# Performance work log

Hardware: AMD Instinct MI355X
Metric: run time of the kernel (lower is better)

## Reference

```python
import jax, jax.numpy as jnp
import numpy as np

B, T = 64, 256
CHAR_V, CHAR_D = 8000, 128
WORD_V, WORD_D = 100000, 300
POS_V, POS_D = 30, 64
SPO_D = 20
D = CHAR_D + WORD_D + POS_D + SPO_D  # 512
L, H, KD, VD, INNER = 4, 8, 64, 64, 2048
C = 25  # num tag classes


def _layer_norm(x, g, b, eps=1e-5):
    m = jnp.mean(x, axis=-1, keepdims=True)
    v = jnp.mean(jnp.square(x - m), axis=-1, keepdims=True)
    return (x - m) * jax.lax.rsqrt(v + eps) * g + b


def setup_inputs() -> dict:
    key = jax.random.key(0)
    ks = jax.random.split(key, 40)
    s = 0.05
    n = lambda k, shp, sc=0.05: jax.random.normal(k, shp, jnp.float32) * sc
    return {
        "char": jax.random.randint(ks[0], (B, T), 0, CHAR_V),
        "word": jax.random.randint(ks[1], (B, T), 0, WORD_V),
        "pos": jax.random.randint(ks[2], (B, T), 0, POS_V),
        "spo": jax.random.normal(ks[3], (B, SPO_D), jnp.float32),
        "seq_len": jax.random.randint(ks[4], (B,), 1, T + 1),
        "tag": jax.random.randint(ks[5], (B, T), 0, C),
        "char_table": n(ks[6], (CHAR_V, CHAR_D)),
        "word_table": n(ks[7], (WORD_V, WORD_D)),
        "pos_table": n(ks[8], (POS_V, POS_D)),
        "ln0_g": jnp.ones((D,), jnp.float32),
        "ln0_b": jnp.zeros((D,), jnp.float32),
        "Wq": n(ks[9], (L, D, H * KD)), "bq": jnp.zeros((L, H * KD), jnp.float32),
        "Wk": n(ks[10], (L, D, H * KD)), "bk": jnp.zeros((L, H * KD), jnp.float32),
        "Wv": n(ks[11], (L, D, H * VD)), "bv": jnp.zeros((L, H * VD), jnp.float32),
        "Wo": n(ks[12], (L, H * VD, D)), "bo": jnp.zeros((L, D), jnp.float32),
        "ln1_g": jnp.ones((L, D), jnp.float32), "ln1_b": jnp.zeros((L, D), jnp.float32),
        "W1": n(ks[13], (L, D, INNER)), "b1": jnp.zeros((L, INNER), jnp.float32),
        "W2": n(ks[14], (L, INNER, D)), "b2": jnp.zeros((L, D), jnp.float32),
        "ln2_g": jnp.ones((L, D), jnp.float32), "ln2_b": jnp.zeros((L, D), jnp.float32),
        "Wout": n(ks[15], (D, C)), "bout": jnp.zeros((C,), jnp.float32),
        "trans": n(ks[16], (C, C)),
    }


def _forward(spo, char_table, word_table, pos_table, ln0_g, ln0_b,
             Wq, bq, Wk, bk, Wv, bv, Wo, bo, ln1_g, ln1_b,
             W1, b1, W2, b2, ln2_g, ln2_b, Wout, bout, trans,
             char, word, pos, seq_len, tag):
    # mask[b,t] = t < seq_len[b]
    mask = (jnp.arange(T)[None, :] < seq_len[:, None]).astype(jnp.float32)  # [B,T]

    # embed + concat + layernorm (dropout in eval mode = identity)
    x = jnp.concatenate([
        char_table[char], word_table[word], pos_table[pos],
        jnp.broadcast_to(spo[:, None, :], (B, T, SPO_D)),
    ], axis=-1)  # [B,T,D]
    x = _layer_norm(x, ln0_g, ln0_b)

    neg_inf = jnp.finfo(x.dtype).min
    key_ok = mask[:, None, None, :] > 0  # [B,1,1,T] key padding mask
    scale = jnp.sqrt(jnp.asarray(KD, x.dtype))
    for l in range(L):
        q = (x @ Wq[l] + bq[l]).reshape(B, T, H, KD).transpose(0, 2, 1, 3)
        k = (x @ Wk[l] + bk[l]).reshape(B, T, H, KD).transpose(0, 2, 1, 3)
        v = (x @ Wv[l] + bv[l]).reshape(B, T, H, VD).transpose(0, 2, 1, 3)
        scores = jnp.einsum('bhqd,bhkd->bhqk', q, k) / scale
        scores = jnp.where(key_ok, scores, neg_inf)
        attn = jax.nn.softmax(scores, axis=-1)
        ctx = jnp.einsum('bhqk,bhkd->bhqd', attn, v).transpose(0, 2, 1, 3).reshape(B, T, H * VD)
        att_out = ctx @ Wo[l] + bo[l]
        h1 = _layer_norm(att_out + x, ln1_g[l], ln1_b[l])
        ff = jax.nn.relu(h1 @ W1[l] + b1[l]) @ W2[l] + b2[l]
        x = _layer_norm(ff + h1, ln2_g[l], ln2_b[l]) * mask[:, :, None]

    logits = x @ Wout + bout  # [B,T,C]

    # ---- CRF negative log likelihood (include_start_end_trans=False) ----
    lg = logits.transpose(1, 0, 2)  # [T,B,C]
    m = mask.T                      # [T,B]

    def step(alpha, inp):
        emit, mt = inp  # emit [B,C], mt [B]
        tmp = alpha[:, :, None] + trans[None, :, :] + emit[:, None, :]  # [B,C,C]
        new = jax.nn.logsumexp(tmp, axis=1)
        alpha = jnp.where(mt[:, None] > 0, new, alpha)
        return alpha, None

    alpha, _ = jax.lax.scan(step, lg[0], (lg[1:], m[1:]))
    log_z = jax.nn.logsumexp(alpha, axis=-1)  # [B]

    tags_t = tag.T  # [T,B]
    emit_gold = jnp.take_along_axis(lg, tags_t[:, :, None], axis=-1)[..., 0] * m  # [T,B]
    trans_gold = trans[tags_t[:-1], tags_t[1:]] * m[1:]  # [T-1,B]
    gold = emit_gold.sum(0) + trans_gold.sum(0)  # [B]

    return jnp.mean(log_z - gold)


def reference(char, word, pos, spo, seq_len, tag, char_table, word_table, pos_table,
              ln0_g, ln0_b, Wq, bq, Wk, bk, Wv, bv, Wo, bo, ln1_g, ln1_b,
              W1, b1, W2, b2, ln2_g, ln2_b, Wout, bout, trans):
    return _forward(spo, char_table, word_table, pos_table, ln0_g, ln0_b,
                    Wq, bq, Wk, bk, Wv, bv, Wo, bo, ln1_g, ln1_b,
                    W1, b1, W2, b2, ln2_g, ln2_b, Wout, bout, trans,
                    char, word, pos, seq_len, tag)
```

## Files before the change

### kernel.cpp

```cpp
#include <hip/hip_runtime.h>
#include <cmath>

namespace {

constexpr int LT = 4;
constexpr int BB = 64;
constexpr int TT = 256;
constexpr int DD = 512;
constexpr int HH = 8;
constexpr int DH = 64;
constexpr int FF = 2048;
constexpr int CC = 25;
constexpr int M_ALL = BB * TT;
constexpr size_t MB = 1024 * 1024;

typedef __attribute__((ext_vector_type(8))) short short8;
typedef __attribute__((ext_vector_type(4))) short short4_;
typedef __attribute__((ext_vector_type(4))) float f32x4;
typedef __attribute__((ext_vector_type(4))) _Float16 half4;

__device__ __forceinline__ float b2f(unsigned short u) {
  union { unsigned int i; float f; } x; x.i = ((unsigned int)u) << 16; return x.f;
}
__device__ __forceinline__ unsigned short f2b(float f) {
  union { float f; unsigned int i; } x; x.f = f;
  unsigned int r = x.i + 0x7FFFu + ((x.i >> 16) & 1u);
  return (unsigned short)(r >> 16);
}
__device__ __forceinline__ float rdlane(float v, int l) {
  union { float f; unsigned int i; } x; x.f = v;
  x.i = (unsigned int)__builtin_amdgcn_readlane((int)x.i, l);
  return x.f;
}
__device__ __forceinline__ void gl_lds16(const void* g, void* l) {
  __builtin_amdgcn_global_load_lds(
      (const __attribute__((address_space(1))) unsigned int*)g,
      (__attribute__((address_space(3))) unsigned int*)l, 16, 0, 0);
}
__device__ __forceinline__ float wredsum(float v) {
#pragma unroll
  for (int o = 32; o > 0; o >>= 1) v += __shfl_xor(v, o, 64);
  return v;
}

__global__ __launch_bounds__(64) void prefix_k(const int* __restrict__ sl,
                                               int* __restrict__ boff) {
  const int l = threadIdx.x;
  int s = sl[l];
#pragma unroll
  for (int o = 1; o < 64; o <<= 1) {
    const int u = __shfl_up(s, o, 64);
    if (l >= o) s += u;
  }
  boff[l + 1] = s;
  if (l == 0) boff[0] = 0;
}

__global__ __launch_bounds__(256) void rowmap_k(const int* __restrict__ sl,
                                                const int* __restrict__ boff,
                                                int* __restrict__ rowmap) {
  const int b = blockIdx.x, t = threadIdx.x;
  if (t < sl[b]) rowmap[boff[b] + t] = (b << 8) | t;
}

template <int NSRC>
__global__ __launch_bounds__(256) void wconv_k(const float* __restrict__ in0,
                                               const float* __restrict__ in1,
                                               const float* __restrict__ in2,
                                               unsigned short* __restrict__ out,
                                               int K, int N, size_t lstride,
                                               size_t sstride) {
  __shared__ float ts[64][65];
  const int k0 = blockIdx.x * 64, n0 = blockIdx.y * 64;
  const float* in = in0;
  if constexpr (NSRC == 3) {
    const int s = blockIdx.z / LT;
    in = (s == 0) ? in0 : (s == 1 ? in1 : in2);
    in += (size_t)(blockIdx.z % LT) * K * N;
    out += (size_t)(blockIdx.z % LT) * lstride + (size_t)(blockIdx.z / LT) * sstride;
  } else {
    in += (size_t)blockIdx.z * K * N;
    out += (size_t)blockIdx.z * lstride;
  }
  const int tid = threadIdx.x;
  for (int i = tid; i < 1024; i += 256) {
    const int r = i >> 4, c4 = i & 15;
    const float4 f = *(const float4*)&in[(size_t)(k0 + r) * N + n0 + c4 * 4];
    ts[r][c4 * 4 + 0] = f.x; ts[r][c4 * 4 + 1] = f.y;
    ts[r][c4 * 4 + 2] = f.z; ts[r][c4 * 4 + 3] = f.w;
  }
  __syncthreads();
  const int n_r = tid >> 2, kc = (tid & 3) * 16;
  short8 v0, v1;
#pragma unroll
  for (int j = 0; j < 8; ++j) {
    v0[j] = (short)f2b(ts[kc + j][n_r]);
    v1[j] = (short)f2b(ts[kc + 8 + j][n_r]);
  }
  unsigned short* op = out + (size_t)(n0 + n_r) * K + k0 + kc;
  *(short8*)op = v0;
  *(short8*)(op + 8) = v1;
}

__global__ __launch_bounds__(256) void embed_ln0_k(
    const int* __restrict__ ch, const int* __restrict__ wd, const int* __restrict__ ps,
    const float* __restrict__ spo, const float* __restrict__ ctab,
    const float* __restrict__ wtab, const float* __restrict__ ptab,
    const float* __restrict__ g, const float* __restrict__ be,
    const int* __restrict__ sl, const int* __restrict__ boff,
    unsigned short* __restrict__ xc) {
  const int row = blockIdx.x * 4 + (threadIdx.x >> 6);
  const int b = row >> 8, t = row & 255;
  if (t >= sl[b]) return;
  const int orow = boff[b] + t;
  const int lane = threadIdx.x & 63;
  const int ci = ch[row], wi = wd[row], pi = ps[row];
  float v[8];
#pragma unroll
  for (int j = 0; j < 2; ++j) {
    const int d = j * 256 + lane * 4;
    float4 f;
    if (d < 128)      f = *(const float4*)&ctab[(size_t)ci * 128 + d];
    else if (d < 428) f = *(const float4*)&wtab[(size_t)wi * 300 + (d - 128)];
    else if (d < 492) f = *(const float4*)&ptab[(size_t)pi * 64 + (d - 428)];
    else              f = *(const float4*)&spo[(size_t)b * 20 + (d - 492)];
    v[j * 4 + 0] = f.x; v[j * 4 + 1] = f.y; v[j * 4 + 2] = f.z; v[j * 4 + 3] = f.w;
  }
  float s = 0.f;
#pragma unroll
  for (int i = 0; i < 8; ++i) s += v[i];
  const float mean = wredsum(s) * (1.0f / 512.0f);
  float vs = 0.f;
#pragma unroll
  for (int i = 0; i < 8; ++i) { const float d = v[i] - mean; vs += d * d; }
  const float rstd = rsqrtf(wredsum(vs) * (1.0f / 512.0f) + 1e-5f);
#pragma unroll
  for (int j = 0; j < 2; ++j) {
    const int d = j * 256 + lane * 4;
    const float4 gv = *(const float4*)&g[d];
    const float4 bv = *(const float4*)&be[d];
    short4_ ob;
    ob[0] = (short)f2b((v[j * 4 + 0] - mean) * rstd * gv.x + bv.x);
    ob[1] = (short)f2b((v[j * 4 + 1] - mean) * rstd * gv.y + bv.y);
    ob[2] = (short)f2b((v[j * 4 + 2] - mean) * rstd * gv.z + bv.z);
    ob[3] = (short)f2b((v[j * 4 + 3] - mean) * rstd * gv.w + bv.w);
    *(short4_*)&xc[(size_t)orow * DD + d] = ob;
  }
}

template <int EPI, int TM>
__global__ __launch_bounds__(256) void gemm_mfma(
    const unsigned short* __restrict__ A, const unsigned short* __restrict__ Bt,
    const float* __restrict__ bias, const float* __restrict__ bias2,
    const float* __restrict__ bias3, const unsigned short* __restrict__ res,
    const int* __restrict__ Mptr, const int* __restrict__ rowmap,
    void* __restrict__ outv, void* __restrict__ out2v, void* __restrict__ out3v,
    int M, int N, int K) {
  constexpr int MI = TM / 32;
  const int Mp = Mptr[0];
  const int m0 = blockIdx.y * TM, n0 = blockIdx.x * 128;
  if (m0 >= Mp) return;
  __shared__ unsigned short As[TM * 64];
  __shared__ unsigned short Bs[128 * 64];
  const int tid = threadIdx.x;
  const int wid = tid >> 6, lane = tid & 63;
  const int wr = wid >> 1, wc = wid & 1;
  const int cl = lane & 15, rg = lane >> 4;
  f32x4 acc[MI][4];
#pragma unroll
  for (int i = 0; i < MI; ++i)
#pragma unroll
    for (int j = 0; j < 4; ++j) acc[i][j] = (f32x4){0.f, 0.f, 0.f, 0.f};

  const int rbase = tid >> 3, sl = tid & 7;
  const int sc = 8 * (sl ^ (rbase & 7));

  for (int k0 = 0; k0 < K; k0 += 64) {
    if (k0) __syncthreads();
#pragma unroll
    for (int i = 0; i < TM / 32; ++i) {
      const int r = i * 32 + rbase;
      gl_lds16(A + (size_t)(m0 + r) * K + k0 + sc, (char*)As + (i * 256 + tid) * 16);
    }
#pragma unroll
    for (int i = 0; i < 4; ++i) {
      const int r = i * 32 + rbase;
      gl_lds16(Bt + (size_t)(n0 + r) * K + k0 + sc, (char*)Bs + (i * 256 + tid) * 16);
    }
    __syncthreads();
#pragma unroll
    for (int ks = 0; ks < 2; ++ks) {
      short8 a[MI], b[4];
      const int kbyte = ks * 64 + rg * 16;
#pragma unroll
      for (int f = 0; f < MI; ++f) {
        const int am = wr * (TM / 2) + f * 16 + cl;
        a[f] = *(const short8*)((const char*)As + am * 128 + (kbyte ^ ((am & 7) << 4)));
      }
#pragma unroll
      for (int f = 0; f < 4; ++f) {
        const int bn = wc * 64 + f * 16 + cl;
        b[f] = *(const short8*)((const char*)Bs + bn * 128 + (kbyte ^ ((bn & 7) << 4)));
      }
#pragma unroll
      for (int mi = 0; mi < MI; ++mi)
#pragma unroll
        for (int ni = 0; ni < 4; ++ni)
          acc[mi][ni] = __builtin_amdgcn_mfma_f32_16x16x32_bf16(a[mi], b[ni],
                                                                acc[mi][ni], 0, 0, 0);
    }
  }

  int rm[MI][4];
  if constexpr (EPI == 5) {
#pragma unroll
    for (int mi = 0; mi < MI; ++mi) {
      const int mb_ = m0 + wr * (TM / 2) + mi * 16 + rg * 4;
#pragma unroll
      for (int i = 0; i < 4; ++i)
        rm[mi][i] = (mb_ + i < Mp) ? rowmap[mb_ + i] : -1;
    }
  }

#pragma unroll
  for (int ni = 0; ni < 4; ++ni) {
    const int n = n0 + wc * 64 + ni * 16 + cl;
    float bv;
    if constexpr (EPI == 5) {
      bv = (n < 512) ? bias[n] : (n < 1024 ? bias2[n - 512] : bias3[n - 1024]);
    } else {
      bv = bias[n];
    }
#pragma unroll
    for (int mi = 0; mi < MI; ++mi) {
      if constexpr (EPI == 5) {
        const int hh = (n >> 6) & 7, d = n & 63;
        if (n < 1024) {
          unsigned short* outp = (unsigned short*)((n < 512) ? outv : out2v);
#pragma unroll
          for (int i = 0; i < 4; ++i) {
            const int rmv = rm[mi][i];
            if (rmv >= 0) {
              const int bb = rmv >> 8, tt = rmv & 255;
              outp[(((size_t)(bb * HH + hh) * TT + tt) << 6) + d] =
                  f2b(acc[mi][ni][i] + bv);
            }
          }
        } else {
          const int rm0 = rm[mi][0];
          if (rm0 >= 0 && rm[mi][3] == rm0 + 3) {
            half4 pk;
#pragma unroll
            for (int i = 0; i < 4; ++i) pk[i] = (_Float16)(acc[mi][ni][i] + bv);
            *(half4*)((_Float16*)out3v +
                      ((((size_t)((rm0 >> 8) * HH + hh) * DH + d) << 8) + (rm0 & 255))) = pk;
          } else {
#pragma unroll
            for (int i = 0; i < 4; ++i) {
              const int rmv = rm[mi][i];
              if (rmv >= 0)
                ((_Float16*)out3v)[(((size_t)((rmv >> 8) * HH + hh) * DH + d) << 8) +
                                   (rmv & 255)] = (_Float16)(acc[mi][ni][i] + bv);
            }
          }
        }
      } else {
#pragma unroll
        for (int i = 0; i < 4; ++i) {
          const int m = m0 + wr * (TM / 2) + mi * 16 + rg * 4 + i;
          const float v = acc[mi][ni][i] + bv;
          if constexpr (EPI == 1) {
            ((unsigned short*)outv)[(size_t)m * N + n] = f2b(fmaxf(v, 0.f));
          } else if constexpr (EPI == 7) {
            ((unsigned short*)outv)[(size_t)m * N + n] =
                f2b(v + b2f(res[(size_t)m * N + n]));
          }
        }
      }
    }
  }
}

__global__ __launch_bounds__(256) void attn_mfma_k(
    const unsigned short* __restrict__ qb, const unsigned short* __restrict__ kbp,
    const _Float16* __restrict__ vtp, const int* __restrict__ seq_len,
    const int* __restrict__ boff, unsigned short* __restrict__ cb) {
  __shared__ unsigned short Ks[256 * 64];
  __shared__ _Float16 Vs[64 * 256];
  __shared__ unsigned short Os[64 * 64];
  const int bh = blockIdx.x;
  const int b = bh >> 3, h = bh & 7;
  const int tid = threadIdx.x;
  const int wid = tid >> 6, lane = tid & 63;
  const int cl = lane & 15, rg = lane >> 4;
  const int len = seq_len[b];
  const int off = boff[b];

  {
    const int r = tid >> 3, sl = tid & 7;
#pragma unroll
    for (int i = 0; i < 8; ++i) {
      if (i * 32 < len) {
        const int row = i * 32 + r;
        gl_lds16(kbp + ((size_t)bh * TT + row) * DH + 8 * (sl ^ (row & 7)),
                 (char*)Ks + (i * 256 + tid) * 16);
      }
    }
#pragma unroll
    for (int i = 0; i < 8; ++i) {
      const int u = i * 256 + tid;
      const int vrow = u >> 5, vsl = u & 31;
      gl_lds16(vtp + ((size_t)bh * DH + vrow) * TT + 8 * (vsl ^ (vrow & 7)),
               (char*)Vs + u * 16);
    }
  }
  __syncthreads();

  for (int qt4 = 0; qt4 < 4; ++qt4) {
    if (qt4 * 64 >= len) break;
    f32x4 o[4];
#pragma unroll
    for (int db = 0; db < 4; ++db) o[db] = (f32x4){0.f, 0.f, 0.f, 0.f};
    {
      const int q0 = qt4 * 64 + wid * 16;
      short8 bqf[2];
      const unsigned short* qp = qb + ((size_t)bh * TT + q0 + cl) * DH + rg * 8;
      bqf[0] = *(const short8*)qp;
      bqf[1] = *(const short8*)(qp + 32);
      f32x4 s[16];
#pragma unroll
      for (int kk = 0; kk < 16; ++kk) {
        s[kk] = (f32x4){0.f, 0.f, 0.f, 0.f};
        if (kk * 16 < len) {
          const int row = kk * 16 + cl;
          const char* base = (const char*)Ks + row * 128;
          const int sw = (row & 7) << 4;
          const short8 a0 = *(const short8*)(base + ((rg * 16) ^ sw));
          const short8 a1 = *(const short8*)(base + ((64 + rg * 16) ^ sw));
          s[kk] = __builtin_amdgcn_mfma_f32_16x16x32_bf16(a0, bqf[0], s[kk], 0, 0, 0);
          s[kk] = __builtin_amdgcn_mfma_f32_16x16x32_bf16(a1, bqf[1], s[kk], 0, 0, 0);
        }
      }
      float mx = -3.0e38f;
#pragma unroll
      for (int kk = 0; kk < 16; ++kk)
        if (kk * 16 < len) {
#pragma unroll
          for (int i = 0; i < 4; ++i) {
            float v = s[kk][i] * 0.125f;
            v = (kk * 16 + rg * 4 + i < len) ? v : -3.0e38f;
            s[kk][i] = v;
            mx = fmaxf(mx, v);
          }
        }
      mx = fmaxf(mx, __shfl_xor(mx, 16, 64));
      mx = fmaxf(mx, __shfl_xor(mx, 32, 64));
      float lsum = 0.f;
#pragma unroll
      for (int kk = 0; kk < 16; ++kk)
        if (kk * 16 < len) {
#pragma unroll
          for (int i = 0; i < 4; ++i) {
            const float p = __expf(s[kk][i] - mx);
            s[kk][i] = p;
            lsum += p;
          }
        }
      lsum += __shfl_xor(lsum, 16, 64);
      lsum += __shfl_xor(lsum, 32, 64);
      const float rl = 1.0f / lsum;
#pragma unroll
      for (int kk = 0; kk < 16; ++kk)
        if (kk * 16 < len) {
          half4 bp;
#pragma unroll
          for (int i = 0; i < 4; ++i) bp[i] = (_Float16)(s[kk][i] * rl);
#pragma unroll
          for (int db = 0; db < 4; ++db) {
            const int vrow = db * 16 + cl;
            const int byte = kk * 32 + rg * 8;
            const half4 a = *(const half4*)((const char*)Vs + vrow * 512 +
                              ((byte & ~15) ^ ((vrow & 7) << 4)) + (byte & 15));
            o[db] = __builtin_amdgcn_mfma_f32_16x16x16f16(a, bp, o[db], 0, 0, 0);
          }
        }
    }
    __syncthreads();
    {
      const int orow = wid * 16 + cl;
      char* obase = (char*)Os + orow * 128;
      const int sw = (orow & 7) << 4;
#pragma unroll
      for (int db = 0; db < 4; ++db) {
        short4_ pk;
#pragma unroll
        for (int i = 0; i < 4; ++i) pk[i] = (short)f2b(o[db][i]);
        const int byte = db * 32 + rg * 8;
        *(short4_*)(obase + ((byte & ~15) ^ sw) + (byte & 15)) = pk;
      }
    }
    __syncthreads();
    {
      const int r = tid >> 2, part = tid & 3;
      const int t = qt4 * 64 + r;
      if (t < len) {
        const int sw = (r & 7) << 4;
        const char* rbase = (const char*)Os + r * 128;
        const short8 w0 = *(const short8*)(rbase + ((part * 32) ^ sw));
        const short8 w1 = *(const short8*)(rbase + ((part * 32 + 16) ^ sw));
        unsigned short* dst = cb + ((size_t)(off + t)) * DD + h * DH + part * 16;
        *(short8*)dst = w0;
        *(short8*)(dst + 8) = w1;
      }
    }
  }
}

__global__ __launch_bounds__(256) void ln_k(const unsigned short* __restrict__ a,
                                            const float* __restrict__ g,
                                            const float* __restrict__ be,
                                            const int* __restrict__ Mptr,
                                            unsigned short* __restrict__ outb) {
  const int row = blockIdx.x * 4 + (threadIdx.x >> 6);
  if (row >= Mptr[0]) return;
  const int lane = threadIdx.x & 63;
  float v[8];
  {
    const short8 va = *(const short8*)&a[(size_t)row * DD + lane * 8];
#pragma unroll
    for (int i = 0; i < 8; ++i) v[i] = b2f((unsigned short)va[i]);
  }
  float s = 0.f;
#pragma unroll
  for (int i = 0; i < 8; ++i) s += v[i];
  const float mean = wredsum(s) * (1.0f / 512.0f);
  float vs = 0.f;
#pragma unroll
  for (int i = 0; i < 8; ++i) { const float d = v[i] - mean; vs += d * d; }
  const float rstd = rsqrtf(wredsum(vs) * (1.0f / 512.0f) + 1e-5f);
  const float4 g0 = *(const float4*)&g[lane * 8];
  const float4 g1 = *(const float4*)&g[lane * 8 + 4];
  const float4 b0 = *(const float4*)&be[lane * 8];
  const float4 b1 = *(const float4*)&be[lane * 8 + 4];
  const float gg[8] = {g0.x, g0.y, g0.z, g0.w, g1.x, g1.y, g1.z, g1.w};
  const float bb[8] = {b0.x, b0.y, b0.z, b0.w, b1.x, b1.y, b1.z, b1.w};
  short8 ob;
#pragma unroll
  for (int i = 0; i < 8; ++i)
    ob[i] = (short)f2b((v[i] - mean) * rstd * gg[i] + bb[i]);
  *(short8*)&outb[(size_t)row * DD + lane * 8] = ob;
}

__global__ __launch_bounds__(256) void logits_k(const unsigned short* __restrict__ xb,
                                                const float* __restrict__ W,
                                                const float* __restrict__ bo,
                                                const int* __restrict__ Mptr,
                                                float* __restrict__ lg) {
  const int r0 = blockIdx.x * 8;
  if (r0 >= Mptr[0]) return;
  __shared__ float xs[8][516];
  for (int i = threadIdx.x; i < 512; i += 256) {
    const int rr = i >> 6, c8 = (i & 63) * 8;
    const short8 v = *(const short8*)&xb[(size_t)(r0 + rr) * DD + c8];
#pragma unroll
    for (int j = 0; j < 8; ++j) xs[rr][c8 + j] = b2f((unsigned short)v[j]);
  }
  __syncthreads();
  const int r = threadIdx.x >> 5, c = threadIdx.x & 31;
  if (c < CC) {
    float acc = 0.f;
#pragma unroll 8
    for (int k = 0; k < DD; ++k) acc += xs[r][k] * W[k * CC + c];
    lg[(size_t)(r0 + r) * CC + c] = acc + bo[c];
  }
}

__global__ __launch_bounds__(64) void crf_k(const float* __restrict__ lg,
                                            const int* __restrict__ tag,
                                            const int* __restrict__ seq_len,
                                            const int* __restrict__ boff,
                                            const float* __restrict__ trans,
                                            float* __restrict__ nll) {
  __shared__ float eexp[TT * CC + 64];
  __shared__ float tr[CC * CC];
  const int b = blockIdx.x;
  const int l = threadIdx.x;
  const int len = seq_len[b];
  const float* lgb = lg + (size_t)boff[b] * CC;
  for (int i = l; i < len * CC; i += 64) eexp[i] = __expf(lgb[i]);
  for (int i = l; i < CC * CC; i += 64) tr[i] = trans[i];
  __syncthreads();
  const int lc = (l < CC) ? l : (CC - 1);
  float et[CC];
#pragma unroll
  for (int i = 0; i < CC; ++i) et[i] = __expf(tr[i * CC + lc]);
  const float e00 = lgb[0];
  float M = e00;
  float A = (l < CC) ? __expf(lgb[l] - e00) : 0.f;
  for (int t = 1; t < len; ++t) {
    const float e = eexp[t * CC + lc];
    float s0 = 0.f, s1 = 0.f, s2 = 0.f, s3 = 0.f, s4 = 0.f;
#pragma unroll
    for (int i = 0; i < CC; i += 5) {
      s0 += rdlane(A, i + 0) * et[i + 0];
      s1 += rdlane(A, i + 1) * et[i + 1];
      s2 += rdlane(A, i + 2) * et[i + 2];
      s3 += rdlane(A, i + 3) * et[i + 3];
      s4 += rdlane(A, i + 4) * et[i + 4];
    }
    A = (((s0 + s1) + (s2 + s3)) + s4) * e;
    if ((t & 3) == 0) {
      const float r = rdlane(A, 0);
      M += __logf(r);
      A *= __builtin_amdgcn_rcpf(r);
    }
  }
  const float tot = wredsum((l < CC) ? A : 0.f);
  float gold = 0.f;
  for (int t = l; t < len; t += 64)
    gold += lgb[t * CC + tag[b * TT + t]];
  for (int t = 1 + l; t < len; t += 64)
    gold += tr[tag[b * TT + t - 1] * CC + tag[b * TT + t]];
  gold = wredsum(gold);
  if (l == 0) nll[b] = (M + __logf(tot)) - gold;
}

__global__ __launch_bounds__(64) void final_k(const float* __restrict__ nll,
                                              float* __restrict__ out) {
  float v = nll[threadIdx.x];
  v = wredsum(v);
  if (threadIdx.x == 0) out[0] = v * (1.0f / 64.0f);
}

}

extern "C" void kernel_launch(void* const* d_in, const int* in_sizes, int n_in,
                              void* d_out, int out_size, void* d_ws, size_t ws_size,
                              hipStream_t stream) {
  (void)in_sizes; (void)n_in; (void)out_size; (void)ws_size;
  const int* chi = (const int*)d_in[0];
  const int* wdi = (const int*)d_in[1];
  const int* psi = (const int*)d_in[2];
  const float* spo = (const float*)d_in[3];
  const int* seq_len = (const int*)d_in[4];
  const int* tag = (const int*)d_in[5];
  const float* ctab = (const float*)d_in[6];
  const float* wtab = (const float*)d_in[7];
  const float* ptab = (const float*)d_in[8];
  const float* ln0g = (const float*)d_in[9];
  const float* ln0b = (const float*)d_in[10];
  const float* Wq = (const float*)d_in[11];
  const float* bq = (const float*)d_in[12];
  const float* Wk = (const float*)d_in[13];
  const float* bk = (const float*)d_in[14];
  const float* Wv = (const float*)d_in[15];
  const float* bv = (const float*)d_in[16];
  const float* Wo = (const float*)d_in[17];
  const float* bo = (const float*)d_in[18];
  const float* ln1g = (const float*)d_in[19];
  const float* ln1b = (const float*)d_in[20];
  const float* W1 = (const float*)d_in[21];
  const float* b1 = (const float*)d_in[22];
  const float* W2 = (const float*)d_in[23];
  const float* b2 = (const float*)d_in[24];
  const float* ln2g = (const float*)d_in[25];
  const float* ln2b = (const float*)d_in[26];
  const float* Wout = (const float*)d_in[27];
  const float* bout = (const float*)d_in[28];
  const float* trans = (const float*)d_in[29];

  char* w8 = (char*)d_ws;
  unsigned short* ib  = (unsigned short*)(w8);
  unsigned short* xc  = (unsigned short*)(w8 + 64 * MB);
  unsigned short* cbx = (unsigned short*)(w8 + 80 * MB);
  unsigned short* ab  = (unsigned short*)(w8 + 96 * MB);
  unsigned short* hb  = (unsigned short*)(w8 + 112 * MB);
  unsigned short* t0b = (unsigned short*)(w8 + 128 * MB);
  unsigned short* qbuf = (unsigned short*)(w8 + 144 * MB);
  unsigned short* kbuf = (unsigned short*)(w8 + 160 * MB);
  _Float16* vtb = (_Float16*)(w8 + 176 * MB);
  unsigned short* wqkv = (unsigned short*)(w8 + 192 * MB);
  unsigned short* wot = (unsigned short*)(w8 + 198 * MB);
  unsigned short* w1t = (unsigned short*)(w8 + 200 * MB);
  unsigned short* w2t = (unsigned short*)(w8 + 208 * MB);
  float* lg = (float*)(w8 + 216 * MB);
  float* nll = (float*)(w8 + 218 * MB);
  int* boff = (int*)(w8 + 219 * MB);
  int* rowmap = (int*)(w8 + 220 * MB);
  const int* Mptr = boff + 64;

  prefix_k<<<1, 64, 0, stream>>>(seq_len, boff);
  rowmap_k<<<BB, 256, 0, stream>>>(seq_len, boff, rowmap);

  const size_t QKVS = (size_t)1536 * 512;
  wconv_k<3><<<dim3(8, 8, 3 * LT), 256, 0, stream>>>(
      Wq, Wk, Wv, wqkv, DD, DD, QKVS, (size_t)512 * 512);
  wconv_k<1><<<dim3(8, 8, LT), 256, 0, stream>>>(
      Wo, nullptr, nullptr, wot, DD, DD, (size_t)DD * DD, 0);
  wconv_k<1><<<dim3(8, 32, LT), 256, 0, stream>>>(
      W1, nullptr, nullptr, w1t, DD, FF, (size_t)DD * FF, 0);
  wconv_k<1><<<dim3(32, 8, LT), 256, 0, stream>>>(
      W2, nullptr, nullptr, w2t, FF, DD, (size_t)FF * DD, 0);

  embed_ln0_k<<<M_ALL / 4, 256, 0, stream>>>(chi, wdi, psi, spo, ctab, wtab, ptab,
                                             ln0g, ln0b, seq_len, boff, xc);

  for (int l = 0; l < LT; ++l) {
    gemm_mfma<5, 64><<<dim3(12, M_ALL / 64), 256, 0, stream>>>(
        xc, wqkv + (size_t)l * QKVS, bq + l * DD, bk + l * DD, bv + l * DD,
        nullptr, Mptr, rowmap, qbuf, kbuf, vtb, M_ALL, 1536, DD);
    attn_mfma_k<<<BB * HH, 256, 0, stream>>>(qbuf, kbuf, vtb, seq_len, boff, cbx);
    gemm_mfma<7, 64><<<dim3(4, M_ALL / 64), 256, 0, stream>>>(
        cbx, wot + (size_t)l * DD * DD, bo + l * DD, nullptr, nullptr,
        xc, Mptr, nullptr, ab, nullptr, nullptr, M_ALL, DD, DD);
    ln_k<<<M_ALL / 4, 256, 0, stream>>>(ab, ln1g + l * DD, ln1b + l * DD, Mptr, hb);
    gemm_mfma<1, 64><<<dim3(FF / 128, M_ALL / 64), 256, 0, stream>>>(
        hb, w1t + (size_t)l * FF * DD, b1 + l * FF, nullptr, nullptr,
        nullptr, Mptr, nullptr, ib, nullptr, nullptr, M_ALL, FF, DD);
    gemm_mfma<7, 64><<<dim3(DD / 128, M_ALL / 64), 256, 0, stream>>>(
        ib, w2t + (size_t)l * FF * DD, b2 + l * DD, nullptr, nullptr,
        hb, Mptr, nullptr, t0b, nullptr, nullptr, M_ALL, DD, FF);
    ln_k<<<M_ALL / 4, 256, 0, stream>>>(t0b, ln2g + l * DD, ln2b + l * DD, Mptr, xc);
  }
  logits_k<<<M_ALL / 8, 256, 0, stream>>>(xc, Wout, bout, Mptr, lg);
  crf_k<<<BB, 64, 0, stream>>>(lg, tag, seq_len, boff, trans, nll);
  final_k<<<1, 64, 0, stream>>>(nll, (float*)d_out);
}
```

Baseline: 842.8 us.

## Double-buffer GEMM LDS, swizzle block order, split attention over query tiles

The GEMM now stages the next K tile into a second LDS buffer while the current tile is computed, which overlaps global loads with MFMA work. Blocks are remapped into grouped M-strips for better L2 reuse of the weight tiles. The QKV and FFN1 GEMMs move to 128-row tiles. The attention kernel is split into one block per (batch, head, 64-query tile), which raises parallelism and skips V columns past the sequence length, at the cost of loading K/V once per query tile. Doubling LDS per block may lower occupancy.

```diff
diff --git a/kernel.cpp b/kernel.cpp
--- a/kernel.cpp
+++ b/kernel.cpp
@@ -158,10 +158,14 @@
     int M, int N, int K) {
   constexpr int MI = TM / 32;
   const int Mp = Mptr[0];
-  const int m0 = blockIdx.y * TM, n0 = blockIdx.x * 128;
+  const int nx = gridDim.x;
+  const int flat = blockIdx.y * nx + blockIdx.x;
+  const int mlo = flat & 7, rr_ = flat >> 3;
+  const int bx = rr_ % nx, by = (rr_ / nx) * 8 + mlo;
+  const int m0 = by * TM, n0 = bx * 128;
   if (m0 >= Mp) return;
-  __shared__ unsigned short As[TM * 64];
-  __shared__ unsigned short Bs[128 * 64];
+  __shared__ unsigned short As[2][TM * 64];
+  __shared__ unsigned short Bs[2][128 * 64];
   const int tid = threadIdx.x;
   const int wid = tid >> 6, lane = tid & 63;
   const int wr = wid >> 1, wc = wid & 1;
@@ -175,19 +179,26 @@
   const int rbase = tid >> 3, sl = tid & 7;
   const int sc = 8 * (sl ^ (rbase & 7));
 
-  for (int k0 = 0; k0 < K; k0 += 64) {
-    if (k0) __syncthreads();
+  auto stage = [&](int buf, int k0) {
 #pragma unroll
     for (int i = 0; i < TM / 32; ++i) {
       const int r = i * 32 + rbase;
-      gl_lds16(A + (size_t)(m0 + r) * K + k0 + sc, (char*)As + (i * 256 + tid) * 16);
+      gl_lds16(A + (size_t)(m0 + r) * K + k0 + sc,
+               (char*)As[buf] + (i * 256 + tid) * 16);
     }
 #pragma unroll
     for (int i = 0; i < 4; ++i) {
       const int r = i * 32 + rbase;
-      gl_lds16(Bt + (size_t)(n0 + r) * K + k0 + sc, (char*)Bs + (i * 256 + tid) * 16);
-    }
-    __syncthreads();
+      gl_lds16(Bt + (size_t)(n0 + r) * K + k0 + sc,
+               (char*)Bs[buf] + (i * 256 + tid) * 16);
+    }
+  };
+
+  stage(0, 0);
+  __syncthreads();
+  int cur = 0;
+  for (int k0 = 0; k0 < K; k0 += 64) {
+    if (k0 + 64 < K) stage(cur ^ 1, k0 + 64);
 #pragma unroll
     for (int ks = 0; ks < 2; ++ks) {
       short8 a[MI], b[4];
@@ -195,12 +206,14 @@
 #pragma unroll
       for (int f = 0; f < MI; ++f) {
         const int am = wr * (TM / 2) + f * 16 + cl;
-        a[f] = *(const short8*)((const char*)As + am * 128 + (kbyte ^ ((am & 7) << 4)));
+        a[f] = *(const short8*)((const char*)As[cur] + am * 128 +
+                                (kbyte ^ ((am & 7) << 4)));
       }
 #pragma unroll
       for (int f = 0; f < 4; ++f) {
         const int bn = wc * 64 + f * 16 + cl;
-        b[f] = *(const short8*)((const char*)Bs + bn * 128 + (kbyte ^ ((bn & 7) << 4)));
+        b[f] = *(const short8*)((const char*)Bs[cur] + bn * 128 +
+                                (kbyte ^ ((bn & 7) << 4)));
       }
 #pragma unroll
       for (int mi = 0; mi < MI; ++mi)
@@ -209,6 +222,8 @@
           acc[mi][ni] = __builtin_amdgcn_mfma_f32_16x16x32_bf16(a[mi], b[ni],
                                                                 acc[mi][ni], 0, 0, 0);
     }
+    __syncthreads();
+    cur ^= 1;
   }
 
   int rm[MI][4];
@@ -288,12 +303,14 @@
   __shared__ unsigned short Ks[256 * 64];
   __shared__ _Float16 Vs[64 * 256];
   __shared__ unsigned short Os[64 * 64];
-  const int bh = blockIdx.x;
+  const int bh = blockIdx.x >> 2;
+  const int qt4 = blockIdx.x & 3;
   const int b = bh >> 3, h = bh & 7;
+  const int len = seq_len[b];
+  if (qt4 * 64 >= len) return;
   const int tid = threadIdx.x;
   const int wid = tid >> 6, lane = tid & 63;
   const int cl = lane & 15, rg = lane >> 4;
-  const int len = seq_len[b];
   const int off = boff[b];
 
   {
@@ -310,108 +327,105 @@
     for (int i = 0; i < 8; ++i) {
       const int u = i * 256 + tid;
       const int vrow = u >> 5, vsl = u & 31;
-      gl_lds16(vtp + ((size_t)bh * DH + vrow) * TT + 8 * (vsl ^ (vrow & 7)),
-               (char*)Vs + u * 16);
+      if (64 * (vsl >> 3) < len)
+        gl_lds16(vtp + ((size_t)bh * DH + vrow) * TT + 8 * (vsl ^ (vrow & 7)),
+                 (char*)Vs + u * 16);
     }
   }
   __syncthreads();
 
-  for (int qt4 = 0; qt4 < 4; ++qt4) {
-    if (qt4 * 64 >= len) break;
-    f32x4 o[4];
-#pragma unroll
-    for (int db = 0; db < 4; ++db) o[db] = (f32x4){0.f, 0.f, 0.f, 0.f};
-    {
-      const int q0 = qt4 * 64 + wid * 16;
-      short8 bqf[2];
-      const unsigned short* qp = qb + ((size_t)bh * TT + q0 + cl) * DH + rg * 8;
-      bqf[0] = *(const short8*)qp;
-      bqf[1] = *(const short8*)(qp + 32);
-      f32x4 s[16];
-#pragma unroll
-      for (int kk = 0; kk < 16; ++kk) {
-        s[kk] = (f32x4){0.f, 0.f, 0.f, 0.f};
-        if (kk * 16 < len) {
-          const int row = kk * 16 + cl;
-          const char* base = (const char*)Ks + row * 128;
-          const int sw = (row & 7) << 4;
-          const short8 a0 = *(const short8*)(base + ((rg * 16) ^ sw));
-          const short8 a1 = *(const short8*)(base + ((64 + rg * 16) ^ sw));
-          s[kk] = __builtin_amdgcn_mfma_f32_16x16x32_bf16(a0, bqf[0], s[kk], 0, 0, 0);
-          s[kk] = __builtin_amdgcn_mfma_f32_16x16x32_bf16(a1, bqf[1], s[kk], 0, 0, 0);
+  f32x4 o[4];
+#pragma unroll
+  for (int db = 0; db < 4; ++db) o[db] = (f32x4){0.f, 0.f, 0.f, 0.f};
+  {
+    const int q0 = qt4 * 64 + wid * 16;
+    short8 bqf[2];
+    const unsigned short* qp = qb + ((size_t)bh * TT + q0 + cl) * DH + rg * 8;
+    bqf[0] = *(const short8*)qp;
+    bqf[1] = *(const short8*)(qp + 32);
+    f32x4 s[16];
+#pragma unroll
+    for (int kk = 0; kk < 16; ++kk) {
+      s[kk] = (f32x4){0.f, 0.f, 0.f, 0.f};
+      if (kk * 16 < len) {
+        const int row = kk * 16 + cl;
+        const char* base = (const char*)Ks + row * 128;
+        const int sw = (row & 7) << 4;
+        const short8 a0 = *(const short8*)(base + ((rg * 16) ^ sw));
+        const short8 a1 = *(const short8*)(base + ((64 + rg * 16) ^ sw));
+        s[kk] = __builtin_amdgcn_mfma_f32_16x16x32_bf16(a0, bqf[0], s[kk], 0, 0, 0);
+        s[kk] = __builtin_amdgcn_mfma_f32_16x16x32_bf16(a1, bqf[1], s[kk], 0, 0, 0);
+      }
+    }
+    float mx = -3.0e38f;
+#pragma unroll
+    for (int kk = 0; kk < 16; ++kk)
+      if (kk * 16 < len) {
+#pragma unroll
+        for (int i = 0; i < 4; ++i) {
+          float v = s[kk][i] * 0.125f;
+          v = (kk * 16 + rg * 4 + i < len) ? v : -3.0e38f;
+          s[kk][i] = v;
+          mx = fmaxf(mx, v);
         }
       }
-      float mx = -3.0e38f;
-#pragma unroll
-      for (int kk = 0; kk < 16; ++kk)
-        if (kk * 16 < len) {
-#pragma unroll
-          for (int i = 0; i < 4; ++i) {
-            float v = s[kk][i] * 0.125f;
-            v = (kk * 16 + rg * 4 + i < len) ? v : -3.0e38f;
-            s[kk][i] = v;
-            mx = fmaxf(mx, v);
-          }
+    mx = fmaxf(mx, __shfl_xor(mx, 16, 64));
+    mx = fmaxf(mx, __shfl_xor(mx, 32, 64));
+    float lsum = 0.f;
+#pragma unroll
+    for (int kk = 0; kk < 16; ++kk)
+      if (kk * 16 < len) {
+#pragma unroll
+        for (int i = 0; i < 4; ++i) {
+          const float p = __expf(s[kk][i] - mx);
+          s[kk][i] = p;
+          lsum += p;
         }
-      mx = fmaxf(mx, __shfl_xor(mx, 16, 64));
-      mx = fmaxf(mx, __shfl_xor(mx, 32, 64));
-      float lsum = 0.f;
-#pragma unroll
-      for (int kk = 0; kk < 16; ++kk)
-        if (kk * 16 < len) {
-#pragma unroll
-          for (int i = 0; i < 4; ++i) {
-            const float p = __expf(s[kk][i] - mx);
-            s[kk][i] = p;
-            lsum += p;
-          }
+      }
+    lsum += __shfl_xor(lsum, 16, 64);
+    lsum += __shfl_xor(lsum, 32, 64);
+    const float rl = 1.0f / lsum;
+#pragma unroll
+    for (int kk = 0; kk < 16; ++kk)
+      if (kk * 16 < len) {
+        half4 bp;
+#pragma unroll
+        for (int i = 0; i < 4; ++i) bp[i] = (_Float16)(s[kk][i] * rl);
+#pragma unroll
+        for (int db = 0; db < 4; ++db) {
+          const int vrow = db * 16 + cl;
+          const int byte = kk * 32 + rg * 8;
+          const half4 a = *(const half4*)((const char*)Vs + vrow * 512 +
+                            ((byte & ~15) ^ ((vrow & 7) << 4)) + (byte & 15));
+          o[db] = __builtin_amdgcn_mfma_f32_16x16x16f16(a, bp, o[db], 0, 0, 0);
         }
-      lsum += __shfl_xor(lsum, 16, 64);
-      lsum += __shfl_xor(lsum, 32, 64);
-      const float rl = 1.0f / lsum;
-#pragma unroll
-      for (int kk = 0; kk < 16; ++kk)
-        if (kk * 16 < len) {
-          half4 bp;
-#pragma unroll
-          for (int i = 0; i < 4; ++i) bp[i] = (_Float16)(s[kk][i] * rl);
-#pragma unroll
-          for (int db = 0; db < 4; ++db) {
-            const int vrow = db * 16 + cl;
-            const int byte = kk * 32 + rg * 8;
-            const half4 a = *(const half4*)((const char*)Vs + vrow * 512 +
-                              ((byte & ~15) ^ ((vrow & 7) << 4)) + (byte & 15));
-            o[db] = __builtin_amdgcn_mfma_f32_16x16x16f16(a, bp, o[db], 0, 0, 0);
-          }
-        }
-    }
-    __syncthreads();
-    {
-      const int orow = wid * 16 + cl;
-      char* obase = (char*)Os + orow * 128;
-      const int sw = (orow & 7) << 4;
-#pragma unroll
-      for (int db = 0; db < 4; ++db) {
-        short4_ pk;
-#pragma unroll
-        for (int i = 0; i < 4; ++i) pk[i] = (short)f2b(o[db][i]);
-        const int byte = db * 32 + rg * 8;
-        *(short4_*)(obase + ((byte & ~15) ^ sw) + (byte & 15)) = pk;
-      }
-    }
-    __syncthreads();
-    {
-      const int r = tid >> 2, part = tid & 3;
-      const int t = qt4 * 64 + r;
-      if (t < len) {
-        const int sw = (r & 7) << 4;
-        const char* rbase = (const char*)Os + r * 128;
-        const short8 w0 = *(const short8*)(rbase + ((part * 32) ^ sw));
-        const short8 w1 = *(const short8*)(rbase + ((part * 32 + 16) ^ sw));
-        unsigned short* dst = cb + ((size_t)(off + t)) * DD + h * DH + part * 16;
-        *(short8*)dst = w0;
-        *(short8*)(dst + 8) = w1;
-      }
+      }
+  }
+  {
+    const int orow = wid * 16 + cl;
+    char* obase = (char*)Os + orow * 128;
+    const int sw = (orow & 7) << 4;
+#pragma unroll
+    for (int db = 0; db < 4; ++db) {
+      short4_ pk;
+#pragma unroll
+      for (int i = 0; i < 4; ++i) pk[i] = (short)f2b(o[db][i]);
+      const int byte = db * 32 + rg * 8;
+      *(short4_*)(obase + ((byte & ~15) ^ sw) + (byte & 15)) = pk;
+    }
+  }
+  __syncthreads();
+  {
+    const int r = tid >> 2, part = tid & 3;
+    const int t = qt4 * 64 + r;
+    if (t < len) {
+      const int sw = (r & 7) << 4;
+      const char* rbase = (const char*)Os + r * 128;
+      const short8 w0 = *(const short8*)(rbase + ((part * 32) ^ sw));
+      const short8 w1 = *(const short8*)(rbase + ((part * 32 + 16) ^ sw));
+      unsigned short* dst = cb + ((size_t)(off + t)) * DD + h * DH + part * 16;
+      *(short8*)dst = w0;
+      *(short8*)(dst + 8) = w1;
     }
   }
 }
@@ -606,18 +620,18 @@
                                              ln0g, ln0b, seq_len, boff, xc);
 
   for (int l = 0; l < LT; ++l) {
-    gemm_mfma<5, 64><<<dim3(12, M_ALL / 64), 256, 0, stream>>>(
+    gemm_mfma<5, 128><<<dim3(12, 128), 256, 0, stream>>>(
         xc, wqkv + (size_t)l * QKVS, bq + l * DD, bk + l * DD, bv + l * DD,
         nullptr, Mptr, rowmap, qbuf, kbuf, vtb, M_ALL, 1536, DD);
-    attn_mfma_k<<<BB * HH, 256, 0, stream>>>(qbuf, kbuf, vtb, seq_len, boff, cbx);
-    gemm_mfma<7, 64><<<dim3(4, M_ALL / 64), 256, 0, stream>>>(
+    attn_mfma_k<<<BB * HH * 4, 256, 0, stream>>>(qbuf, kbuf, vtb, seq_len, boff, cbx);
+    gemm_mfma<7, 64><<<dim3(4, 256), 256, 0, stream>>>(
         cbx, wot + (size_t)l * DD * DD, bo + l * DD, nullptr, nullptr,
         xc, Mptr, nullptr, ab, nullptr, nullptr, M_ALL, DD, DD);
     ln_k<<<M_ALL / 4, 256, 0, stream>>>(ab, ln1g + l * DD, ln1b + l * DD, Mptr, hb);
-    gemm_mfma<1, 64><<<dim3(FF / 128, M_ALL / 64), 256, 0, stream>>>(
+    gemm_mfma<1, 128><<<dim3(FF / 128, 128), 256, 0, stream>>>(
         hb, w1t + (size_t)l * FF * DD, b1 + l * FF, nullptr, nullptr,
         nullptr, Mptr, nullptr, ib, nullptr, nullptr, M_ALL, FF, DD);
-    gemm_mfma<7, 64><<<dim3(DD / 128, M_ALL / 64), 256, 0, stream>>>(
+    gemm_mfma<7, 64><<<dim3(4, 256), 256, 0, stream>>>(
         ib, w2t + (size_t)l * FF * DD, b2 + l * DD, nullptr, nullptr,
         hb, Mptr, nullptr, t0b, nullptr, nullptr, M_ALL, DD, FF);
     ln_k<<<M_ALL / 4, 256, 0, stream>>>(t0b, ln2g + l * DD, ln2b + l * DD, Mptr, xc);
```

New measurement: 768.7 us. 8.8% less time.
